# Optimization experiments

Measured on AMD Instinct MI355X. Metric: run time of the kernel, lower is better.

The kernel has to match this reference:

```python
import jax, jax.numpy as jnp
import numpy as np

N = 50000
E = 800000
B = 64
NODE_IN, EDGE_IN, H, OUT_DIM = 16, 8, 64, 2


def _glorot(key, shape):
    fan_in, fan_out = shape[0], shape[-1]
    s = jnp.sqrt(6.0 / (fan_in + fan_out))
    return jax.random.uniform(key, shape, jnp.float32, -s, s)


def setup_inputs() -> dict:
    key = jax.random.key(0)
    ks = jax.random.split(key, 32)
    inp = {
        'x': jax.random.normal(ks[0], (N, NODE_IN), jnp.float32),
        'edge_index': jax.random.randint(ks[1], (2, E), 0, N).astype(jnp.int64),
        'edge_attr': jax.random.normal(ks[2], (E, EDGE_IN), jnp.float32),
        'batch': jnp.sort(jax.random.randint(ks[3], (N,), 0, B)).astype(jnp.int64),
        # encoders
        'W_node': _glorot(ks[4], (NODE_IN, H)), 'b_node': jnp.zeros((H,), jnp.float32),
        'W_edge': _glorot(ks[5], (EDGE_IN, H)), 'b_edge': jnp.zeros((H,), jnp.float32),
        # conv1: GATv2, heads=4, concat=True, edge_dim=H
        'Wl1': _glorot(ks[6], (H, 4 * H)), 'bl1': jnp.zeros((4 * H,), jnp.float32),
        'Wr1': _glorot(ks[7], (H, 4 * H)), 'br1': jnp.zeros((4 * H,), jnp.float32),
        'We1': _glorot(ks[8], (H, 4 * H)),
        'att1': _glorot(ks[9], (4, H)),
        'bias1': jnp.zeros((4 * H,), jnp.float32),
        # conv2: GATv2, heads=1, concat=False, in=4H
        'Wl2': _glorot(ks[10], (4 * H, H)), 'bl2': jnp.zeros((H,), jnp.float32),
        'Wr2': _glorot(ks[11], (4 * H, H)), 'br2': jnp.zeros((H,), jnp.float32),
        'We2': _glorot(ks[12], (H, H)),
        'att2': _glorot(ks[13], (1, H)),
        'bias2': jnp.zeros((H,), jnp.float32),
        # decoder
        'Wd1': _glorot(ks[14], (H, H)), 'bd1': jnp.zeros((H,), jnp.float32),
        'Wd2': _glorot(ks[15], (H, OUT_DIM)), 'bd2': jnp.zeros((OUT_DIM,), jnp.float32),
    }
    return inp


def _gatv2(x, src, dst, eattr, Wl, bl, Wr, br, We, att, bias, heads, out_ch, concat):
    n = x.shape[0]
    # add self-loops with edge_attr fill_value='mean' (segment mean over dst), PyG default
    ones = jnp.ones((src.shape[0],), x.dtype)
    deg = jax.ops.segment_sum(ones, dst, num_segments=n)
    loop_attr = jax.ops.segment_sum(eattr, dst, num_segments=n) / jnp.clip(deg, 1.0)[:, None]
    ea = jnp.concatenate([eattr, loop_attr], 0)               # [E+N, F_e]
    s = jnp.concatenate([src, jnp.arange(n)], 0)
    d = jnp.concatenate([dst, jnp.arange(n)], 0)
    xl = (x @ Wl + bl).reshape(n, heads, out_ch)              # source transform
    xr = (x @ Wr + br).reshape(n, heads, out_ch)              # target transform
    ep = (ea @ We).reshape(-1, heads, out_ch)                 # edge transform (no bias)
    m = jax.nn.leaky_relu(xl[s] + xr[d] + ep, 0.2)            # [E+N, heads, out_ch]
    logits = jnp.einsum('ehc,hc->eh', m, att)
    lmax = jax.ops.segment_max(logits, d, num_segments=n)
    lmax = jnp.where(jnp.isfinite(lmax), lmax, 0.0)
    a = jnp.exp(logits - lmax[d])
    denom = jax.ops.segment_sum(a, d, num_segments=n)
    alpha = a / (denom[d] + 1e-16)                            # segment softmax over dst
    out = jax.ops.segment_sum(alpha[..., None] * xl[s], d, num_segments=n)
    out = out.reshape(n, heads * out_ch) if concat else out.mean(1)
    return out + bias


def reference(x, edge_index, edge_attr, batch, W_node, b_node, W_edge, b_edge,
              Wl1, bl1, Wr1, br1, We1, att1, bias1,
              Wl2, bl2, Wr2, br2, We2, att2, bias2,
              Wd1, bd1, Wd2, bd2):
    src, dst = edge_index[0], edge_index[1]
    h = x @ W_node + b_node
    ea = edge_attr @ W_edge + b_edge
    h = jax.nn.elu(_gatv2(h, src, dst, ea, Wl1, bl1, Wr1, br1, We1, att1, bias1, 4, H, True))
    h = _gatv2(h, src, dst, ea, Wl2, bl2, Wr2, br2, We2, att2, bias2, 1, H, False)
    # global mean pool over batch vector
    cnt = jax.ops.segment_sum(jnp.ones((h.shape[0],), h.dtype), batch, num_segments=B)
    pooled = jax.ops.segment_sum(h, batch, num_segments=B) / jnp.clip(cnt, 1.0)[:, None]
    out = jax.nn.relu(pooled @ Wd1 + bd1) @ Wd2 + bd2
    return jax.nn.sigmoid(out)
```

## Files before the change

kernel.cpp:

```cpp
#include <hip/hip_runtime.h>
#include <math.h>

#define NN 50000
#define NE 800000
#define NB 64

__device__ __forceinline__ int permpos(int c) {
  return ((c & 63) << 2) | (((c >> 6) ^ c) & 3);
}

__device__ __forceinline__ unsigned short f2bf(float f) {
  unsigned int u = __float_as_uint(f);
  u += 0x7fffu + ((u >> 16) & 1u);
  return (unsigned short)(u >> 16);
}
__device__ __forceinline__ float bf2f(unsigned short b) {
  return __uint_as_float(((unsigned int)b) << 16);
}

__global__ void k_zero(int* __restrict__ p, int n) {
  int i = blockIdx.x * blockDim.x + threadIdx.x;
  if (i < n) p[i] = 0;
}

__global__ void k_fuse(const float* __restrict__ Wn, const float* __restrict__ bn,
                       const float* __restrict__ We, const float* __restrict__ be,
                       const float* __restrict__ Wl1, const float* __restrict__ bl1,
                       const float* __restrict__ Wr1, const float* __restrict__ br1,
                       const float* __restrict__ We1, const float* __restrict__ We2,
                       const float* __restrict__ att1, const float* __restrict__ bias1,
                       float* __restrict__ wl1e, float* __restrict__ bl1e,
                       float* __restrict__ wr1e, float* __restrict__ br1e,
                       float* __restrict__ wfe1, float* __restrict__ bfe1,
                       float* __restrict__ wfe2, float* __restrict__ bfe2,
                       float* __restrict__ att1p, float* __restrict__ bias1p) {
  int t = blockIdx.x * blockDim.x + threadIdx.x;
  if (t < 4096) {
    int i = t >> 8, j = t & 255; float s = 0.f;
    for (int k = 0; k < 64; k++) s += Wn[i * 64 + k] * Wl1[k * 256 + j];
    wl1e[i * 256 + permpos(j)] = s;
  } else if (t < 8192) {
    int u = t - 4096; int i = u >> 8, j = u & 255; float s = 0.f;
    for (int k = 0; k < 64; k++) s += Wn[i * 64 + k] * Wr1[k * 256 + j];
    wr1e[i * 256 + permpos(j)] = s;
  } else if (t < 10240) {
    int u = t - 8192; int i = u >> 8, j = u & 255; float s = 0.f;
    for (int k = 0; k < 64; k++) s += We[i * 64 + k] * We1[k * 256 + j];
    wfe1[i * 256 + permpos(j)] = s;
  } else if (t < 10752) {
    int u = t - 10240; int i = u >> 6, j = u & 63; float s = 0.f;
    for (int k = 0; k < 64; k++) s += We[i * 64 + k] * We2[k * 64 + j];
    wfe2[u] = s;
  } else if (t < 11008) {
    int j = t - 10752; float s = bl1[j];
    for (int k = 0; k < 64; k++) s += bn[k] * Wl1[k * 256 + j];
    bl1e[permpos(j)] = s;
  } else if (t < 11264) {
    int j = t - 11008; float s = br1[j];
    for (int k = 0; k < 64; k++) s += bn[k] * Wr1[k * 256 + j];
    br1e[permpos(j)] = s;
  } else if (t < 11520) {
    int j = t - 11264; float s = 0.f;
    for (int k = 0; k < 64; k++) s += be[k] * We1[k * 256 + j];
    bfe1[permpos(j)] = s;
  } else if (t < 11584) {
    int j = t - 11520; float s = 0.f;
    for (int k = 0; k < 64; k++) s += be[k] * We2[k * 64 + j];
    bfe2[j] = s;
  } else if (t < 11840) {
    int j = t - 11584;
    att1p[permpos(j)] = att1[j];
  } else if (t < 12096) {
    int j = t - 11840;
    bias1p[permpos(j)] = bias1[j];
  }
}

__global__ void k_deg(const int* __restrict__ dstA, int* __restrict__ deg) {
  int e = blockIdx.x * blockDim.x + threadIdx.x;
  if (e < NE) atomicAdd(&deg[dstA[e]], 1);
}

__global__ __launch_bounds__(1024) void k_scan1(const int* __restrict__ deg,
                                                int* __restrict__ incl, int* __restrict__ partials) {
  __shared__ int sm[1024];
  int i = blockIdx.x * 1024 + threadIdx.x;
  int v = (i < NN) ? (deg[i] + 1) : 0;
  sm[threadIdx.x] = v;
  __syncthreads();
  for (int off = 1; off < 1024; off <<= 1) {
    int t = (threadIdx.x >= off) ? sm[threadIdx.x - off] : 0;
    __syncthreads();
    sm[threadIdx.x] += t;
    __syncthreads();
  }
  if (i < NN) incl[i] = sm[threadIdx.x];
  if (threadIdx.x == 1023) partials[blockIdx.x] = sm[1023];
}

__global__ void k_scan2(int* __restrict__ partials, int* __restrict__ rowptr, int nblk) {
  int t = threadIdx.x;
  int v = (t < nblk) ? partials[t] : 0;
  for (int off = 1; off < 64; off <<= 1) {
    int u = __shfl_up(v, off, 64);
    if (t >= off) v += u;
  }
  if (t < nblk) partials[t] = v;
  if (t == nblk - 1) rowptr[NN] = v;
}

__global__ void k_scan3(const int* __restrict__ deg, const int* __restrict__ incl,
                        const int* __restrict__ partials, int* __restrict__ rowptr) {
  int i = blockIdx.x * blockDim.x + threadIdx.x;
  if (i >= NN) return;
  int blk = i >> 10;
  int base = blk ? partials[blk - 1] : 0;
  rowptr[i] = base + incl[i] - (deg[i] + 1);
}

__global__ void k_csr(const int* __restrict__ srcA, const int* __restrict__ dstA,
                      const int* __restrict__ rowptr, const int* __restrict__ deg,
                      int* __restrict__ cursor, int2* __restrict__ csr) {
  int t = blockIdx.x * blockDim.x + threadIdx.x;
  if (t < NE) {
    int d = dstA[t];
    int pos = rowptr[d] + atomicAdd(&cursor[d], 1);
    csr[pos] = make_int2(t, srcA[t]);
  } else if (t < NE + NN) {
    int n = t - NE;
    csr[rowptr[n] + deg[n]] = make_int2(NE + n, n);
  }
}

__global__ __launch_bounds__(256) void k_loop8(const int* __restrict__ rowptr,
                                               const int2* __restrict__ csr,
                                               const float* __restrict__ eattr,
                                               float* __restrict__ lattr) {
  int d = (blockIdx.x * blockDim.x + threadIdx.x) >> 6;
  int lane = threadIdx.x & 63;
  if (d >= NN) return;
  int beg = rowptr[d], endReal = rowptr[d + 1] - 1;
  int k = lane & 7, sub = lane >> 3;
  float s = 0.f;
  for (int i = beg + sub; i < endReal; i += 8) {
    int eid = csr[i].x;
    s += eattr[(size_t)eid * 8 + k];
  }
  s += __shfl_xor(s, 8, 64);
  s += __shfl_xor(s, 16, 64);
  s += __shfl_xor(s, 32, 64);
  float invdeg = 1.f / fmaxf((float)(endReal - beg), 1.f);
  if (lane < 8) lattr[(size_t)d * 8 + lane] = s * invdeg;
}

__global__ __launch_bounds__(256) void k_lin1(const float* __restrict__ x,
                                              const float* __restrict__ wl, const float* __restrict__ bl,
                                              const float* __restrict__ wr, const float* __restrict__ br,
                                              unsigned short* __restrict__ xl, float* __restrict__ xr) {
  __shared__ float xs[4][16];
  int nb = blockIdx.x * 4;
  int t = threadIdx.x;
  if (t < 64) xs[t >> 4][t & 15] = x[nb * 16 + t];
  __syncthreads();
  int w = t >> 6, lane = t & 63, l4 = lane << 2;
  float4 accl = *(const float4*)(bl + l4);
  float4 accr = *(const float4*)(br + l4);
  const float* xrow = xs[w];
#pragma unroll
  for (int k = 0; k < 16; k++) {
    float xv = xrow[k];
    float4 wl4 = *(const float4*)(wl + k * 256 + l4);
    float4 wr4 = *(const float4*)(wr + k * 256 + l4);
    accl.x += xv * wl4.x; accl.y += xv * wl4.y; accl.z += xv * wl4.z; accl.w += xv * wl4.w;
    accr.x += xv * wr4.x; accr.y += xv * wr4.y; accr.z += xv * wr4.z; accr.w += xv * wr4.w;
  }
  int node = nb + w;
  ushort4 us;
  us.x = f2bf(accl.x); us.y = f2bf(accl.y); us.z = f2bf(accl.z); us.w = f2bf(accl.w);
  *(ushort4*)(xl + (size_t)node * 256 + l4) = us;
  *(float4*)(xr + (size_t)node * 256 + l4) = accr;
}

__device__ __forceinline__ const float* ek_ptr(const float* __restrict__ eattr,
                                               const float* __restrict__ lattr, int eid) {
  return (eid < NE) ? (eattr + (size_t)eid * 8) : (lattr + (size_t)(eid - NE) * 8);
}

__device__ __forceinline__ float jreduce(float part[4]) {
  part[0] += __shfl_xor(part[1], 1, 64);
  part[2] += __shfl_xor(part[3], 1, 64);
  float v = part[0] + __shfl_xor(part[2], 2, 64);
  v += __shfl_xor(v, 4, 64);
  v += __shfl_xor(v, 8, 64);
  v += __shfl_xor(v, 16, 64);
  v += __shfl_xor(v, 32, 64);
  return v;
}

__global__ __launch_bounds__(256) void k_conv1(
    const float* __restrict__ eattr, const float* __restrict__ lattr,
    const int* __restrict__ rowptr, const int2* __restrict__ csr,
    const unsigned short* __restrict__ xl, const float* __restrict__ xrg,
    const float* __restrict__ att1p, const float* __restrict__ bias1p,
    const float* __restrict__ wfe1, const float* __restrict__ bfe1,
    float* __restrict__ out1) {
  int d = __builtin_amdgcn_readfirstlane((blockIdx.x * blockDim.x + threadIdx.x) >> 6);
  int lane = threadIdx.x & 63;
  if (d >= NN) return;
  int l4 = lane << 2;
  float4 xr4 = *(const float4*)(xrg + (size_t)d * 256 + l4);
  float4 at4 = *(const float4*)(att1p + l4);
  float4 bf4 = *(const float4*)(bfe1 + l4);
  float4 wf[8];
#pragma unroll
  for (int k = 0; k < 8; k++) wf[k] = *(const float4*)(wfe1 + k * 256 + l4);

  float acc0 = 0.f, acc1 = 0.f, acc2 = 0.f, acc3 = 0.f;
  float mrun = -INFINITY, lrun = 0.f;
  int beg = rowptr[d], end = rowptr[d + 1];

  auto ld4 = [&](int s) -> float4 {
    ushort4 u = *(const ushort4*)(xl + (size_t)s * 256 + l4);
    float4 f; f.x = bf2f(u.x); f.y = bf2f(u.y); f.z = bf2f(u.z); f.w = bf2f(u.w);
    return f;
  };
  auto epart = [&](const float* __restrict__ p, const float4& x4, float part[4]) {
    float e0 = bf4.x, e1 = bf4.y, e2 = bf4.z, e3 = bf4.w;
#pragma unroll
    for (int k = 0; k < 8; k++) {
      float ekv = p[k];
      e0 += ekv * wf[k].x; e1 += ekv * wf[k].y;
      e2 += ekv * wf[k].z; e3 += ekv * wf[k].w;
    }
    float m0 = x4.x + xr4.x + e0; m0 = (m0 > 0.f) ? m0 : 0.2f * m0;
    float m1 = x4.y + xr4.y + e1; m1 = (m1 > 0.f) ? m1 : 0.2f * m1;
    float m2 = x4.z + xr4.z + e2; m2 = (m2 > 0.f) ? m2 : 0.2f * m2;
    float m3 = x4.w + xr4.w + e3; m3 = (m3 > 0.f) ? m3 : 0.2f * m3;
    part[0] = at4.x * m0; part[1] = at4.y * m1;
    part[2] = at4.z * m2; part[3] = at4.w * m3;
  };

  int idx = beg;
  for (; idx + 4 <= end; idx += 4) {
    int2 e0 = csr[idx], e1 = csr[idx + 1], e2 = csr[idx + 2], e3 = csr[idx + 3];
    int s0 = __builtin_amdgcn_readfirstlane(e0.y), id0 = __builtin_amdgcn_readfirstlane(e0.x);
    int s1 = __builtin_amdgcn_readfirstlane(e1.y), id1 = __builtin_amdgcn_readfirstlane(e1.x);
    int s2 = __builtin_amdgcn_readfirstlane(e2.y), id2 = __builtin_amdgcn_readfirstlane(e2.x);
    int s3 = __builtin_amdgcn_readfirstlane(e3.y), id3 = __builtin_amdgcn_readfirstlane(e3.x);
    float4 x0 = ld4(s0), x1 = ld4(s1), x2 = ld4(s2), x3 = ld4(s3);
    float pa[4], pb[4], pc[4], pd[4];
    epart(ek_ptr(eattr, lattr, id0), x0, pa);
    epart(ek_ptr(eattr, lattr, id1), x1, pb);
    epart(ek_ptr(eattr, lattr, id2), x2, pc);
    epart(ek_ptr(eattr, lattr, id3), x3, pd);
    float v0 = jreduce(pa), v1 = jreduce(pb), v2 = jreduce(pc), v3 = jreduce(pd);
    float gmax = fmaxf(fmaxf(v0, v1), fmaxf(v2, v3));
    if (__ballot(gmax > mrun)) {
      float nm = fmaxf(mrun, gmax);
      float sc = __expf(mrun - nm);
      mrun = nm; lrun *= sc;
      float sc1 = __shfl_xor(sc, 1, 64);
      float sc2 = __shfl_xor(sc, 2, 64);
      float sc3 = __shfl_xor(sc1, 2, 64);
      acc0 *= sc; acc1 *= sc1; acc2 *= sc2; acc3 *= sc3;
    }
    float q0 = __expf(v0 - mrun), q1 = __expf(v1 - mrun);
    float q2 = __expf(v2 - mrun), q3 = __expf(v3 - mrun);
    lrun += q0 + q1 + q2 + q3;
    {
      float a1 = __shfl_xor(q0, 1, 64), a2 = __shfl_xor(q0, 2, 64), a3 = __shfl_xor(a1, 2, 64);
      acc0 += q0 * x0.x; acc1 += a1 * x0.y; acc2 += a2 * x0.z; acc3 += a3 * x0.w;
    }
    {
      float a1 = __shfl_xor(q1, 1, 64), a2 = __shfl_xor(q1, 2, 64), a3 = __shfl_xor(a1, 2, 64);
      acc0 += q1 * x1.x; acc1 += a1 * x1.y; acc2 += a2 * x1.z; acc3 += a3 * x1.w;
    }
    {
      float a1 = __shfl_xor(q2, 1, 64), a2 = __shfl_xor(q2, 2, 64), a3 = __shfl_xor(a1, 2, 64);
      acc0 += q2 * x2.x; acc1 += a1 * x2.y; acc2 += a2 * x2.z; acc3 += a3 * x2.w;
    }
    {
      float a1 = __shfl_xor(q3, 1, 64), a2 = __shfl_xor(q3, 2, 64), a3 = __shfl_xor(a1, 2, 64);
      acc0 += q3 * x3.x; acc1 += a1 * x3.y; acc2 += a2 * x3.z; acc3 += a3 * x3.w;
    }
  }
  for (; idx < end; ++idx) {
    int2 e0 = csr[idx];
    int s0 = __builtin_amdgcn_readfirstlane(e0.y), id0 = __builtin_amdgcn_readfirstlane(e0.x);
    float4 x0 = ld4(s0);
    float pa[4];
    epart(ek_ptr(eattr, lattr, id0), x0, pa);
    float v0 = jreduce(pa);
    if (__ballot(v0 > mrun)) {
      float nm = fmaxf(mrun, v0);
      float sc = __expf(mrun - nm);
      mrun = nm; lrun *= sc;
      float sc1 = __shfl_xor(sc, 1, 64);
      float sc2 = __shfl_xor(sc, 2, 64);
      float sc3 = __shfl_xor(sc1, 2, 64);
      acc0 *= sc; acc1 *= sc1; acc2 *= sc2; acc3 *= sc3;
    }
    float q0 = __expf(v0 - mrun);
    lrun += q0;
    float a1 = __shfl_xor(q0, 1, 64), a2 = __shfl_xor(q0, 2, 64), a3 = __shfl_xor(a1, 2, 64);
    acc0 += q0 * x0.x; acc1 += a1 * x0.y; acc2 += a2 * x0.z; acc3 += a3 * x0.w;
  }

  float lr0 = lrun;
  float lr1 = __shfl_xor(lr0, 1, 64);
  float lr2 = __shfl_xor(lr0, 2, 64);
  float lr3 = __shfl_xor(lr1, 2, 64);
  float4 bi4 = *(const float4*)(bias1p + l4);
  float4 o;
  o.x = acc0 / (lr0 + 1e-16f) + bi4.x;
  o.y = acc1 / (lr1 + 1e-16f) + bi4.y;
  o.z = acc2 / (lr2 + 1e-16f) + bi4.z;
  o.w = acc3 / (lr3 + 1e-16f) + bi4.w;
  o.x = (o.x > 0.f) ? o.x : (__expf(o.x) - 1.f);
  o.y = (o.y > 0.f) ? o.y : (__expf(o.y) - 1.f);
  o.z = (o.z > 0.f) ? o.z : (__expf(o.z) - 1.f);
  o.w = (o.w > 0.f) ? o.w : (__expf(o.w) - 1.f);
  *(float4*)(out1 + (size_t)d * 256 + l4) = o;
}

__global__ __launch_bounds__(256) void k_lin2(const float* __restrict__ in,
                                              const float* __restrict__ wl, const float* __restrict__ bl,
                                              const float* __restrict__ wr, const float* __restrict__ br,
                                              unsigned short* __restrict__ xl, float* __restrict__ xr) {
  int col = threadIdx.x & 63;
  int grp = threadIdx.x >> 6;
  int node0 = blockIdx.x * 32 + grp * 8;
  float sl[8], sr[8];
  float blv = bl[col], brv = br[col];
#pragma unroll
  for (int u = 0; u < 8; u++) { sl[u] = blv; sr[u] = brv; }
  const float4* r[8];
#pragma unroll
  for (int u = 0; u < 8; u++) r[u] = (const float4*)(in + (size_t)(node0 + u) * 256);
#pragma unroll 2
  for (int g4 = 0; g4 < 64; g4++) {
    int b = g4 & 3;
    int i0 = ((0 ^ b) << 6) + g4;
    int i1 = ((1 ^ b) << 6) + g4;
    int i2 = ((2 ^ b) << 6) + g4;
    int i3 = ((3 ^ b) << 6) + g4;
    float wl0 = wl[i0 * 64 + col], wl1v = wl[i1 * 64 + col];
    float wl2v = wl[i2 * 64 + col], wl3v = wl[i3 * 64 + col];
    float wr0 = wr[i0 * 64 + col], wr1v = wr[i1 * 64 + col];
    float wr2v = wr[i2 * 64 + col], wr3v = wr[i3 * 64 + col];
#pragma unroll
    for (int u = 0; u < 8; u++) {
      float4 v = r[u][g4];
      sl[u] += v.x * wl0 + v.y * wl1v + v.z * wl2v + v.w * wl3v;
      sr[u] += v.x * wr0 + v.y * wr1v + v.z * wr2v + v.w * wr3v;
    }
  }
#pragma unroll
  for (int u = 0; u < 8; u++) {
    int node = node0 + u;
    if (node < NN) {
      xl[(size_t)node * 64 + col] = f2bf(sl[u]);
      xr[(size_t)node * 64 + col] = sr[u];
    }
  }
}

__global__ __launch_bounds__(256) void k_conv2(
    const float* __restrict__ eattr, const float* __restrict__ lattr,
    const int* __restrict__ rowptr, const int2* __restrict__ csr,
    const unsigned short* __restrict__ xl, const float* __restrict__ xrg,
    const float* __restrict__ att2, const float* __restrict__ bias2,
    const float* __restrict__ wfe2, const float* __restrict__ bfe2,
    float* __restrict__ out2) {
  int d = __builtin_amdgcn_readfirstlane((blockIdx.x * blockDim.x + threadIdx.x) >> 6);
  int lane = threadIdx.x & 63;
  if (d >= NN) return;
  float xr_l = xrg[(size_t)d * 64 + lane];
  float att_l = att2[lane];
  float bfe_l = bfe2[lane];
  float wfe_l[8];
#pragma unroll
  for (int k = 0; k < 8; k++) wfe_l[k] = wfe2[k * 64 + lane];
  float acc = 0.f, mrun = -INFINITY, lrun = 0.f;
  int beg = rowptr[d], end = rowptr[d + 1];
  bool b0 = (lane & 1), b1 = (lane & 2);

  auto pl = [&](const float* __restrict__ p, float xs) {
    float ep = bfe_l;
#pragma unroll
    for (int k = 0; k < 8; k++) ep += p[k] * wfe_l[k];
    float m = xs + xr_l + ep;
    m = (m > 0.f) ? m : 0.2f * m;
    return att_l * m;
  };

  int idx = beg;
  for (; idx + 4 <= end; idx += 4) {
    int2 e0 = csr[idx], e1 = csr[idx + 1], e2 = csr[idx + 2], e3 = csr[idx + 3];
    int s0 = __builtin_amdgcn_readfirstlane(e0.y), id0 = __builtin_amdgcn_readfirstlane(e0.x);
    int s1 = __builtin_amdgcn_readfirstlane(e1.y), id1 = __builtin_amdgcn_readfirstlane(e1.x);
    int s2 = __builtin_amdgcn_readfirstlane(e2.y), id2 = __builtin_amdgcn_readfirstlane(e2.x);
    int s3 = __builtin_amdgcn_readfirstlane(e3.y), id3 = __builtin_amdgcn_readfirstlane(e3.x);
    float x0 = bf2f(xl[(size_t)s0 * 64 + lane]);
    float x1 = bf2f(xl[(size_t)s1 * 64 + lane]);
    float x2 = bf2f(xl[(size_t)s2 * 64 + lane]);
    float x3 = bf2f(xl[(size_t)s3 * 64 + lane]);
    float v0 = pl(ek_ptr(eattr, lattr, id0), x0);
    float v1 = pl(ek_ptr(eattr, lattr, id1), x1);
    float v2 = pl(ek_ptr(eattr, lattr, id2), x2);
    float v3 = pl(ek_ptr(eattr, lattr, id3), x3);
    float a01 = b0 ? v1 : v0;
    a01 += __shfl_xor(b0 ? v0 : v1, 1, 64);
    float a23 = b0 ? v3 : v2;
    a23 += __shfl_xor(b0 ? v2 : v3, 1, 64);
    float w = b1 ? a23 : a01;
    w += __shfl_xor(b1 ? a01 : a23, 2, 64);
    w += __shfl_xor(w, 4, 64);
    w += __shfl_xor(w, 8, 64);
    w += __shfl_xor(w, 16, 64);
    w += __shfl_xor(w, 32, 64);
    float g = fmaxf(w, __shfl_xor(w, 1, 64));
    g = fmaxf(g, __shfl_xor(g, 2, 64));
    if (g > mrun) {
      float sc = __expf(mrun - g);
      mrun = g; lrun *= sc; acc *= sc;
    }
    float q = __expf(w - mrun);
    float q1 = __shfl_xor(q, 1, 64);
    float q2 = __shfl_xor(q, 2, 64);
    float q3 = __shfl_xor(q1, 2, 64);
    lrun += (q + q1) + (q2 + q3);
    float u01 = b0 ? x1 : x0, u10 = b0 ? x0 : x1;
    float u23 = b0 ? x3 : x2, u32 = b0 ? x2 : x3;
    float xr0 = b1 ? u23 : u01;
    float xr1v = b1 ? u32 : u10;
    float xr2v = b1 ? u01 : u23;
    float xr3v = b1 ? u10 : u32;
    acc += q * xr0 + q1 * xr1v + q2 * xr2v + q3 * xr3v;
  }
  for (; idx < end; ++idx) {
    int2 e0 = csr[idx];
    int s0 = __builtin_amdgcn_readfirstlane(e0.y), id0 = __builtin_amdgcn_readfirstlane(e0.x);
    float x0 = bf2f(xl[(size_t)s0 * 64 + lane]);
    float v = pl(ek_ptr(eattr, lattr, id0), x0);
    v += __shfl_xor(v, 1, 64);
    v += __shfl_xor(v, 2, 64);
    v += __shfl_xor(v, 4, 64);
    v += __shfl_xor(v, 8, 64);
    v += __shfl_xor(v, 16, 64);
    v += __shfl_xor(v, 32, 64);
    if (v > mrun) {
      float sc = __expf(mrun - v);
      mrun = v; lrun *= sc; acc *= sc;
    }
    float q = __expf(v - mrun);
    lrun += q;
    acc += q * x0;
  }
  out2[(size_t)d * 64 + lane] = acc / (lrun + 1e-16f) + bias2[lane];
}

__device__ __forceinline__ int lowerb(const int* a, int n, int v) {
  int lo = 0, hi = n;
  while (lo < hi) {
    int mid = (lo + hi) >> 1;
    if (a[mid] < v) lo = mid + 1; else hi = mid;
  }
  return lo;
}

__global__ __launch_bounds__(256) void k_pool(const int* __restrict__ batch,
                                              const float* __restrict__ out2,
                                              float* __restrict__ pooled) {
  int b = blockIdx.x;
  int start = lowerb(batch, NN, b);
  int end = lowerb(batch, NN, b + 1);
  int c = threadIdx.x & 63, sub = threadIdx.x >> 6;
  float s = 0.f;
  for (int i = start + sub; i < end; i += 4) s += out2[(size_t)i * 64 + c];
  __shared__ float sm[256];
  sm[threadIdx.x] = s;
  __syncthreads();
  if (sub == 0) {
    float tot = sm[c] + sm[64 + c] + sm[128 + c] + sm[192 + c];
    float cnt = fmaxf((float)(end - start), 1.f);
    pooled[b * 64 + c] = tot / cnt;
  }
}

__global__ __launch_bounds__(1024) void k_dec(const float* __restrict__ pooled,
                                              const float* __restrict__ Wd1, const float* __restrict__ bd1,
                                              const float* __restrict__ Wd2, const float* __restrict__ bd2,
                                              float* __restrict__ out) {
  __shared__ float hid[64 * 64];
  int t = threadIdx.x;
  for (int i = t; i < 4096; i += 1024) {
    int b = i >> 6, j = i & 63;
    float s = bd1[j];
#pragma unroll 8
    for (int k = 0; k < 64; k++) s += pooled[b * 64 + k] * Wd1[k * 64 + j];
    hid[i] = fmaxf(s, 0.f);
  }
  __syncthreads();
  if (t < 128) {
    int b = t >> 1, o = t & 1;
    float s = bd2[o];
#pragma unroll 8
    for (int k = 0; k < 64; k++) s += hid[b * 64 + k] * Wd2[k * 2 + o];
    out[t] = 1.f / (1.f + __expf(-s));
  }
}

extern "C" void kernel_launch(void* const* d_in, const int* in_sizes, int n_in,
                              void* d_out, int out_size, void* d_ws, size_t ws_size,
                              hipStream_t stream) {
  const float* x     = (const float*)d_in[0];
  const int*   eidx  = (const int*)d_in[1];
  const float* eattr = (const float*)d_in[2];
  const int*   batch = (const int*)d_in[3];
  const float* Wn    = (const float*)d_in[4];
  const float* bn    = (const float*)d_in[5];
  const float* We    = (const float*)d_in[6];
  const float* be    = (const float*)d_in[7];
  const float* Wl1   = (const float*)d_in[8];
  const float* bl1   = (const float*)d_in[9];
  const float* Wr1   = (const float*)d_in[10];
  const float* br1   = (const float*)d_in[11];
  const float* We1   = (const float*)d_in[12];
  const float* att1  = (const float*)d_in[13];
  const float* bias1 = (const float*)d_in[14];
  const float* Wl2   = (const float*)d_in[15];
  const float* bl2   = (const float*)d_in[16];
  const float* Wr2   = (const float*)d_in[17];
  const float* br2   = (const float*)d_in[18];
  const float* We2   = (const float*)d_in[19];
  const float* att2  = (const float*)d_in[20];
  const float* bias2 = (const float*)d_in[21];
  const float* Wd1   = (const float*)d_in[22];
  const float* bd1   = (const float*)d_in[23];
  const float* Wd2   = (const float*)d_in[24];
  const float* bd2   = (const float*)d_in[25];

  const int* srcA = eidx;
  const int* dstA = eidx + NE;

  char* ws = (char*)d_ws;
  size_t off = 0;
  auto alloc = [&](size_t bytes) -> char* {
    char* p = ws + off;
    off += (bytes + 255) & ~(size_t)255;
    return p;
  };

  int*   deg    = (int*)alloc(NN * 4);
  int*   cursor = (int*)alloc(NN * 4);
  size_t zero_bytes = off;
  int*   rowptr   = (int*)alloc((NN + 1) * 4);
  int*   incl     = (int*)alloc(NN * 4);
  int*   partials = (int*)alloc(64 * 4);
  int2*  csr      = (int2*)alloc((size_t)(NE + NN + 1) * 8);
  float* lattr = (float*)alloc((size_t)NN * 8 * 4);
  float* wl1e  = (float*)alloc(4096 * 4);
  float* wr1e  = (float*)alloc(4096 * 4);
  float* wfe1  = (float*)alloc(2048 * 4);
  float* wfe2  = (float*)alloc(512 * 4);
  float* bl1e  = (float*)alloc(256 * 4);
  float* br1e  = (float*)alloc(256 * 4);
  float* bfe1  = (float*)alloc(256 * 4);
  float* bfe2  = (float*)alloc(64 * 4);
  float* att1p = (float*)alloc(256 * 4);
  float* bias1p= (float*)alloc(256 * 4);
  unsigned short* xl1 = (unsigned short*)alloc((size_t)NN * 256 * 2);
  float* xr1   = (float*)alloc((size_t)NN * 256 * 4);
  float* out1  = (float*)alloc((size_t)NN * 256 * 4);
  unsigned short* xl2 = (unsigned short*)alloc((size_t)NN * 64 * 2);
  float* xr2   = (float*)alloc((size_t)NN * 64 * 4);
  float* out2  = (float*)alloc((size_t)NN * 64 * 4);
  float* pooled = (float*)alloc((size_t)NB * 64 * 4);

  int zn = (int)(zero_bytes / 4);
  int nscan = (NN + 1023) / 1024;
  k_zero<<<(zn + 255) / 256, 256, 0, stream>>>((int*)d_ws, zn);
  k_fuse<<<(12096 + 255) / 256, 256, 0, stream>>>(Wn, bn, We, be, Wl1, bl1, Wr1, br1, We1, We2,
                                                  att1, bias1,
                                                  wl1e, bl1e, wr1e, br1e, wfe1, bfe1, wfe2, bfe2,
                                                  att1p, bias1p);
  k_deg<<<(NE + 255) / 256, 256, 0, stream>>>(dstA, deg);
  k_scan1<<<nscan, 1024, 0, stream>>>(deg, incl, partials);
  k_scan2<<<1, 64, 0, stream>>>(partials, rowptr, nscan);
  k_scan3<<<(NN + 255) / 256, 256, 0, stream>>>(deg, incl, partials, rowptr);
  k_csr<<<(NE + NN + 255) / 256, 256, 0, stream>>>(srcA, dstA, rowptr, deg, cursor, csr);
  k_loop8<<<(NN + 3) / 4, 256, 0, stream>>>(rowptr, csr, eattr, lattr);
  k_lin1<<<NN / 4, 256, 0, stream>>>(x, wl1e, bl1e, wr1e, br1e, xl1, xr1);
  k_conv1<<<(NN + 3) / 4, 256, 0, stream>>>(eattr, lattr, rowptr, csr, xl1, xr1,
                                            att1p, bias1p, wfe1, bfe1, out1);
  k_lin2<<<(NN + 31) / 32, 256, 0, stream>>>(out1, Wl2, bl2, Wr2, br2, xl2, xr2);
  k_conv2<<<(NN + 3) / 4, 256, 0, stream>>>(eattr, lattr, rowptr, csr, xl2, xr2,
                                            att2, bias2, wfe2, bfe2, out2);
  k_pool<<<NB, 256, 0, stream>>>(batch, out2, pooled);
  k_dec<<<1, 1024, 0, stream>>>(pooled, Wd1, bd1, Wd2, bd2, (float*)d_out);
}
```

Baseline: 771.7 us.

## Split GATv2 convs into per-edge logit kernels and per-node softmax aggregation

Attention logits are now computed in separate edge-parallel kernels (one wave per four CSR entries, reading a new per-position dst array) and written to buffers. The per-node aggregation kernels then only read precomputed logits plus gathered source features. This is meant to spread the heavy per-edge work evenly instead of binding it to skewed per-node loops. Edge biases are folded into the right-projection biases, and attention vectors are pre-scaled by log2(e) so exp2f can be used. The cost is extra logit and dst buffers, plus a second gather of x_l in the logit pass.

Result: slower. 894.4 us (+15.9%).

```diff
diff --git a/kernel.cpp b/kernel.cpp
--- a/kernel.cpp
+++ b/kernel.cpp
@@ -4,6 +4,8 @@
 #define NN 50000
 #define NE 800000
 #define NB 64
+#define TOT 850000
+#define LOG2E 1.4426950408889634f
 
 __device__ __forceinline__ int permpos(int c) {
   return ((c & 63) << 2) | (((c >> 6) ^ c) & 3);
@@ -29,11 +31,13 @@
                        const float* __restrict__ Wr1, const float* __restrict__ br1,
                        const float* __restrict__ We1, const float* __restrict__ We2,
                        const float* __restrict__ att1, const float* __restrict__ bias1,
+                       const float* __restrict__ att2,
                        float* __restrict__ wl1e, float* __restrict__ bl1e,
                        float* __restrict__ wr1e, float* __restrict__ br1e,
-                       float* __restrict__ wfe1, float* __restrict__ bfe1,
-                       float* __restrict__ wfe2, float* __restrict__ bfe2,
-                       float* __restrict__ att1p, float* __restrict__ bias1p) {
+                       float* __restrict__ wfe1, float* __restrict__ wfe2,
+                       float* __restrict__ bfe2,
+                       float* __restrict__ att1p, float* __restrict__ att2p,
+                       float* __restrict__ bias1p) {
   int t = blockIdx.x * blockDim.x + threadIdx.x;
   if (t < 4096) {
     int i = t >> 8, j = t & 255; float s = 0.f;
@@ -58,20 +62,20 @@
   } else if (t < 11264) {
     int j = t - 11008; float s = br1[j];
     for (int k = 0; k < 64; k++) s += bn[k] * Wr1[k * 256 + j];
+    for (int k = 0; k < 64; k++) s += be[k] * We1[k * 256 + j];
     br1e[permpos(j)] = s;
-  } else if (t < 11520) {
+  } else if (t < 11328) {
     int j = t - 11264; float s = 0.f;
-    for (int k = 0; k < 64; k++) s += be[k] * We1[k * 256 + j];
-    bfe1[permpos(j)] = s;
-  } else if (t < 11584) {
-    int j = t - 11520; float s = 0.f;
     for (int k = 0; k < 64; k++) s += be[k] * We2[k * 64 + j];
     bfe2[j] = s;
-  } else if (t < 11840) {
+  } else if (t < 11584) {
+    int j = t - 11328;
+    att1p[permpos(j)] = att1[j] * LOG2E;
+  } else if (t < 11648) {
     int j = t - 11584;
-    att1p[permpos(j)] = att1[j];
-  } else if (t < 12096) {
-    int j = t - 11840;
+    att2p[j] = att2[j] * LOG2E;
+  } else if (t < 11904) {
+    int j = t - 11648;
     bias1p[permpos(j)] = bias1[j];
   }
 }
@@ -120,15 +124,19 @@
 
 __global__ void k_csr(const int* __restrict__ srcA, const int* __restrict__ dstA,
                       const int* __restrict__ rowptr, const int* __restrict__ deg,
-                      int* __restrict__ cursor, int2* __restrict__ csr) {
+                      int* __restrict__ cursor, int2* __restrict__ csr,
+                      int* __restrict__ dstp) {
   int t = blockIdx.x * blockDim.x + threadIdx.x;
   if (t < NE) {
     int d = dstA[t];
     int pos = rowptr[d] + atomicAdd(&cursor[d], 1);
     csr[pos] = make_int2(t, srcA[t]);
+    dstp[pos] = d;
   } else if (t < NE + NN) {
     int n = t - NE;
-    csr[rowptr[n] + deg[n]] = make_int2(NE + n, n);
+    int pos = rowptr[n] + deg[n];
+    csr[pos] = make_int2(NE + n, n);
+    dstp[pos] = n;
   }
 }
 
@@ -197,24 +205,66 @@
   return v;
 }
 
-__global__ __launch_bounds__(256) void k_conv1(
+__global__ __launch_bounds__(256) void k_elogit1(
     const float* __restrict__ eattr, const float* __restrict__ lattr,
+    const int2* __restrict__ csr, const int* __restrict__ dstp,
+    const unsigned short* __restrict__ xl, const float* __restrict__ xrb,
+    const float* __restrict__ att1p, const float* __restrict__ wfe1,
+    float* __restrict__ logit1) {
+  int wid = (blockIdx.x * blockDim.x + threadIdx.x) >> 6;
+  int lane = threadIdx.x & 63;
+  int p0 = wid * 4;
+  int l4 = lane << 2;
+  float4 at4 = *(const float4*)(att1p + l4);
+  float4 wf[8];
+#pragma unroll
+  for (int k = 0; k < 8; k++) wf[k] = *(const float4*)(wfe1 + k * 256 + l4);
+  float v[4];
+#pragma unroll
+  for (int i = 0; i < 4; i++) {
+    int p = p0 + i;
+    int2 e = csr[p];
+    int eid = __builtin_amdgcn_readfirstlane(e.x);
+    int s   = __builtin_amdgcn_readfirstlane(e.y);
+    int dd  = __builtin_amdgcn_readfirstlane(dstp[p]);
+    const float* ekp = ek_ptr(eattr, lattr, eid);
+    float4 xb = *(const float4*)(xrb + (size_t)dd * 256 + l4);
+    ushort4 u = *(const ushort4*)(xl + (size_t)s * 256 + l4);
+    float m0 = xb.x + bf2f(u.x);
+    float m1 = xb.y + bf2f(u.y);
+    float m2 = xb.z + bf2f(u.z);
+    float m3 = xb.w + bf2f(u.w);
+#pragma unroll
+    for (int k = 0; k < 8; k++) {
+      float ekv = ekp[k];
+      m0 += ekv * wf[k].x; m1 += ekv * wf[k].y;
+      m2 += ekv * wf[k].z; m3 += ekv * wf[k].w;
+    }
+    m0 = (m0 > 0.f) ? m0 : 0.2f * m0;
+    m1 = (m1 > 0.f) ? m1 : 0.2f * m1;
+    m2 = (m2 > 0.f) ? m2 : 0.2f * m2;
+    m3 = (m3 > 0.f) ? m3 : 0.2f * m3;
+    float part[4] = {at4.x * m0, at4.y * m1, at4.z * m2, at4.w * m3};
+    v[i] = jreduce(part);
+  }
+  int key = (lane >> 2) & 3;
+  float a = (key & 1) ? v[1] : v[0];
+  float b = (key & 1) ? v[3] : v[2];
+  float out = (key & 2) ? b : a;
+  if (lane < 16) logit1[(size_t)p0 * 4 + lane] = out;
+}
+
+__global__ __launch_bounds__(256) void k_conv1l(
     const int* __restrict__ rowptr, const int2* __restrict__ csr,
-    const unsigned short* __restrict__ xl, const float* __restrict__ xrg,
-    const float* __restrict__ att1p, const float* __restrict__ bias1p,
-    const float* __restrict__ wfe1, const float* __restrict__ bfe1,
+    const float* __restrict__ logit1,
+    const unsigned short* __restrict__ xl,
+    const float* __restrict__ bias1p,
     float* __restrict__ out1) {
   int d = __builtin_amdgcn_readfirstlane((blockIdx.x * blockDim.x + threadIdx.x) >> 6);
   int lane = threadIdx.x & 63;
   if (d >= NN) return;
   int l4 = lane << 2;
-  float4 xr4 = *(const float4*)(xrg + (size_t)d * 256 + l4);
-  float4 at4 = *(const float4*)(att1p + l4);
-  float4 bf4 = *(const float4*)(bfe1 + l4);
-  float4 wf[8];
-#pragma unroll
-  for (int k = 0; k < 8; k++) wf[k] = *(const float4*)(wfe1 + k * 256 + l4);
-
+  int k = lane & 3;
   float acc0 = 0.f, acc1 = 0.f, acc2 = 0.f, acc3 = 0.f;
   float mrun = -INFINITY, lrun = 0.f;
   int beg = rowptr[d], end = rowptr[d + 1];
@@ -224,49 +274,36 @@
     float4 f; f.x = bf2f(u.x); f.y = bf2f(u.y); f.z = bf2f(u.z); f.w = bf2f(u.w);
     return f;
   };
-  auto epart = [&](const float* __restrict__ p, const float4& x4, float part[4]) {
-    float e0 = bf4.x, e1 = bf4.y, e2 = bf4.z, e3 = bf4.w;
-#pragma unroll
-    for (int k = 0; k < 8; k++) {
-      float ekv = p[k];
-      e0 += ekv * wf[k].x; e1 += ekv * wf[k].y;
-      e2 += ekv * wf[k].z; e3 += ekv * wf[k].w;
-    }
-    float m0 = x4.x + xr4.x + e0; m0 = (m0 > 0.f) ? m0 : 0.2f * m0;
-    float m1 = x4.y + xr4.y + e1; m1 = (m1 > 0.f) ? m1 : 0.2f * m1;
-    float m2 = x4.z + xr4.z + e2; m2 = (m2 > 0.f) ? m2 : 0.2f * m2;
-    float m3 = x4.w + xr4.w + e3; m3 = (m3 > 0.f) ? m3 : 0.2f * m3;
-    part[0] = at4.x * m0; part[1] = at4.y * m1;
-    part[2] = at4.z * m2; part[3] = at4.w * m3;
+  auto sel = [&](const float4& lg) -> float {
+    float a = (k & 1) ? lg.y : lg.x;
+    float b = (k & 1) ? lg.w : lg.z;
+    return (k & 2) ? b : a;
   };
 
   int idx = beg;
   for (; idx + 4 <= end; idx += 4) {
     int2 e0 = csr[idx], e1 = csr[idx + 1], e2 = csr[idx + 2], e3 = csr[idx + 3];
-    int s0 = __builtin_amdgcn_readfirstlane(e0.y), id0 = __builtin_amdgcn_readfirstlane(e0.x);
-    int s1 = __builtin_amdgcn_readfirstlane(e1.y), id1 = __builtin_amdgcn_readfirstlane(e1.x);
-    int s2 = __builtin_amdgcn_readfirstlane(e2.y), id2 = __builtin_amdgcn_readfirstlane(e2.x);
-    int s3 = __builtin_amdgcn_readfirstlane(e3.y), id3 = __builtin_amdgcn_readfirstlane(e3.x);
+    int s0 = __builtin_amdgcn_readfirstlane(e0.y);
+    int s1 = __builtin_amdgcn_readfirstlane(e1.y);
+    int s2 = __builtin_amdgcn_readfirstlane(e2.y);
+    int s3 = __builtin_amdgcn_readfirstlane(e3.y);
+    const float4* lgp = (const float4*)(logit1 + (size_t)idx * 4);
+    float4 lg0 = lgp[0], lg1 = lgp[1], lg2 = lgp[2], lg3 = lgp[3];
+    float v0 = sel(lg0), v1 = sel(lg1), v2 = sel(lg2), v3 = sel(lg3);
     float4 x0 = ld4(s0), x1 = ld4(s1), x2 = ld4(s2), x3 = ld4(s3);
-    float pa[4], pb[4], pc[4], pd[4];
-    epart(ek_ptr(eattr, lattr, id0), x0, pa);
-    epart(ek_ptr(eattr, lattr, id1), x1, pb);
-    epart(ek_ptr(eattr, lattr, id2), x2, pc);
-    epart(ek_ptr(eattr, lattr, id3), x3, pd);
-    float v0 = jreduce(pa), v1 = jreduce(pb), v2 = jreduce(pc), v3 = jreduce(pd);
     float gmax = fmaxf(fmaxf(v0, v1), fmaxf(v2, v3));
     if (__ballot(gmax > mrun)) {
       float nm = fmaxf(mrun, gmax);
-      float sc = __expf(mrun - nm);
+      float sc = exp2f(mrun - nm);
       mrun = nm; lrun *= sc;
       float sc1 = __shfl_xor(sc, 1, 64);
       float sc2 = __shfl_xor(sc, 2, 64);
       float sc3 = __shfl_xor(sc1, 2, 64);
       acc0 *= sc; acc1 *= sc1; acc2 *= sc2; acc3 *= sc3;
     }
-    float q0 = __expf(v0 - mrun), q1 = __expf(v1 - mrun);
-    float q2 = __expf(v2 - mrun), q3 = __expf(v3 - mrun);
-    lrun += q0 + q1 + q2 + q3;
+    float q0 = exp2f(v0 - mrun), q1 = exp2f(v1 - mrun);
+    float q2 = exp2f(v2 - mrun), q3 = exp2f(v3 - mrun);
+    lrun += (q0 + q1) + (q2 + q3);
     {
       float a1 = __shfl_xor(q0, 1, 64), a2 = __shfl_xor(q0, 2, 64), a3 = __shfl_xor(a1, 2, 64);
       acc0 += q0 * x0.x; acc1 += a1 * x0.y; acc2 += a2 * x0.z; acc3 += a3 * x0.w;
@@ -286,21 +323,20 @@
   }
   for (; idx < end; ++idx) {
     int2 e0 = csr[idx];
-    int s0 = __builtin_amdgcn_readfirstlane(e0.y), id0 = __builtin_amdgcn_readfirstlane(e0.x);
+    int s0 = __builtin_amdgcn_readfirstlane(e0.y);
+    float4 lg0 = *(const float4*)(logit1 + (size_t)idx * 4);
+    float v0 = sel(lg0);
     float4 x0 = ld4(s0);
-    float pa[4];
-    epart(ek_ptr(eattr, lattr, id0), x0, pa);
-    float v0 = jreduce(pa);
     if (__ballot(v0 > mrun)) {
       float nm = fmaxf(mrun, v0);
-      float sc = __expf(mrun - nm);
+      float sc = exp2f(mrun - nm);
       mrun = nm; lrun *= sc;
       float sc1 = __shfl_xor(sc, 1, 64);
       float sc2 = __shfl_xor(sc, 2, 64);
       float sc3 = __shfl_xor(sc1, 2, 64);
       acc0 *= sc; acc1 *= sc1; acc2 *= sc2; acc3 *= sc3;
     }
-    float q0 = __expf(v0 - mrun);
+    float q0 = exp2f(v0 - mrun);
     lrun += q0;
     float a1 = __shfl_xor(q0, 1, 64), a2 = __shfl_xor(q0, 2, 64), a3 = __shfl_xor(a1, 2, 64);
     acc0 += q0 * x0.x; acc1 += a1 * x0.y; acc2 += a2 * x0.z; acc3 += a3 * x0.w;
@@ -326,12 +362,13 @@
 __global__ __launch_bounds__(256) void k_lin2(const float* __restrict__ in,
                                               const float* __restrict__ wl, const float* __restrict__ bl,
                                               const float* __restrict__ wr, const float* __restrict__ br,
+                                              const float* __restrict__ bfe2,
                                               unsigned short* __restrict__ xl, float* __restrict__ xr) {
   int col = threadIdx.x & 63;
   int grp = threadIdx.x >> 6;
   int node0 = blockIdx.x * 32 + grp * 8;
   float sl[8], sr[8];
-  float blv = bl[col], brv = br[col];
+  float blv = bl[col], brv = br[col] + bfe2[col];
 #pragma unroll
   for (int u = 0; u < 8; u++) { sl[u] = blv; sr[u] = brv; }
   const float4* r[8];
@@ -365,95 +402,92 @@
   }
 }
 
-__global__ __launch_bounds__(256) void k_conv2(
+__global__ __launch_bounds__(256) void k_elogit2(
     const float* __restrict__ eattr, const float* __restrict__ lattr,
+    const int2* __restrict__ csr, const int* __restrict__ dstp,
+    const unsigned short* __restrict__ xl, const float* __restrict__ xrb,
+    const float* __restrict__ att2p, const float* __restrict__ wfe2,
+    float* __restrict__ logit2) {
+  int wid = (blockIdx.x * blockDim.x + threadIdx.x) >> 6;
+  int lane = threadIdx.x & 63;
+  int p0 = wid * 4;
+  float att_l = att2p[lane];
+  float wfe_l[8];
+#pragma unroll
+  for (int k = 0; k < 8; k++) wfe_l[k] = wfe2[k * 64 + lane];
+  float v[4];
+#pragma unroll
+  for (int i = 0; i < 4; i++) {
+    int p = p0 + i;
+    int2 e = csr[p];
+    int eid = __builtin_amdgcn_readfirstlane(e.x);
+    int s   = __builtin_amdgcn_readfirstlane(e.y);
+    int dd  = __builtin_amdgcn_readfirstlane(dstp[p]);
+    const float* ekp = ek_ptr(eattr, lattr, eid);
+    float m = xrb[(size_t)dd * 64 + lane] + bf2f(xl[(size_t)s * 64 + lane]);
+#pragma unroll
+    for (int k = 0; k < 8; k++) m += ekp[k] * wfe_l[k];
+    m = (m > 0.f) ? m : 0.2f * m;
+    float t = att_l * m;
+    t += __shfl_xor(t, 1, 64);
+    t += __shfl_xor(t, 2, 64);
+    t += __shfl_xor(t, 4, 64);
+    t += __shfl_xor(t, 8, 64);
+    t += __shfl_xor(t, 16, 64);
+    t += __shfl_xor(t, 32, 64);
+    v[i] = t;
+  }
+  int key = lane & 3;
+  float a = (key & 1) ? v[1] : v[0];
+  float b = (key & 1) ? v[3] : v[2];
+  float out = (key & 2) ? b : a;
+  if (lane < 4) logit2[p0 + lane] = out;
+}
+
+__global__ __launch_bounds__(256) void k_conv2l(
     const int* __restrict__ rowptr, const int2* __restrict__ csr,
-    const unsigned short* __restrict__ xl, const float* __restrict__ xrg,
-    const float* __restrict__ att2, const float* __restrict__ bias2,
-    const float* __restrict__ wfe2, const float* __restrict__ bfe2,
+    const float* __restrict__ logit2,
+    const unsigned short* __restrict__ xl,
+    const float* __restrict__ bias2,
     float* __restrict__ out2) {
   int d = __builtin_amdgcn_readfirstlane((blockIdx.x * blockDim.x + threadIdx.x) >> 6);
   int lane = threadIdx.x & 63;
   if (d >= NN) return;
-  float xr_l = xrg[(size_t)d * 64 + lane];
-  float att_l = att2[lane];
-  float bfe_l = bfe2[lane];
-  float wfe_l[8];
-#pragma unroll
-  for (int k = 0; k < 8; k++) wfe_l[k] = wfe2[k * 64 + lane];
   float acc = 0.f, mrun = -INFINITY, lrun = 0.f;
   int beg = rowptr[d], end = rowptr[d + 1];
-  bool b0 = (lane & 1), b1 = (lane & 2);
-
-  auto pl = [&](const float* __restrict__ p, float xs) {
-    float ep = bfe_l;
-#pragma unroll
-    for (int k = 0; k < 8; k++) ep += p[k] * wfe_l[k];
-    float m = xs + xr_l + ep;
-    m = (m > 0.f) ? m : 0.2f * m;
-    return att_l * m;
-  };
 
   int idx = beg;
   for (; idx + 4 <= end; idx += 4) {
     int2 e0 = csr[idx], e1 = csr[idx + 1], e2 = csr[idx + 2], e3 = csr[idx + 3];
-    int s0 = __builtin_amdgcn_readfirstlane(e0.y), id0 = __builtin_amdgcn_readfirstlane(e0.x);
-    int s1 = __builtin_amdgcn_readfirstlane(e1.y), id1 = __builtin_amdgcn_readfirstlane(e1.x);
-    int s2 = __builtin_amdgcn_readfirstlane(e2.y), id2 = __builtin_amdgcn_readfirstlane(e2.x);
-    int s3 = __builtin_amdgcn_readfirstlane(e3.y), id3 = __builtin_amdgcn_readfirstlane(e3.x);
+    int s0 = __builtin_amdgcn_readfirstlane(e0.y);
+    int s1 = __builtin_amdgcn_readfirstlane(e1.y);
+    int s2 = __builtin_amdgcn_readfirstlane(e2.y);
+    int s3 = __builtin_amdgcn_readfirstlane(e3.y);
+    float l0 = logit2[idx], l1 = logit2[idx + 1], l2 = logit2[idx + 2], l3 = logit2[idx + 3];
     float x0 = bf2f(xl[(size_t)s0 * 64 + lane]);
     float x1 = bf2f(xl[(size_t)s1 * 64 + lane]);
     float x2 = bf2f(xl[(size_t)s2 * 64 + lane]);
     float x3 = bf2f(xl[(size_t)s3 * 64 + lane]);
-    float v0 = pl(ek_ptr(eattr, lattr, id0), x0);
-    float v1 = pl(ek_ptr(eattr, lattr, id1), x1);
-    float v2 = pl(ek_ptr(eattr, lattr, id2), x2);
-    float v3 = pl(ek_ptr(eattr, lattr, id3), x3);
-    float a01 = b0 ? v1 : v0;
-    a01 += __shfl_xor(b0 ? v0 : v1, 1, 64);
-    float a23 = b0 ? v3 : v2;
-    a23 += __shfl_xor(b0 ? v2 : v3, 1, 64);
-    float w = b1 ? a23 : a01;
-    w += __shfl_xor(b1 ? a01 : a23, 2, 64);
-    w += __shfl_xor(w, 4, 64);
-    w += __shfl_xor(w, 8, 64);
-    w += __shfl_xor(w, 16, 64);
-    w += __shfl_xor(w, 32, 64);
-    float g = fmaxf(w, __shfl_xor(w, 1, 64));
-    g = fmaxf(g, __shfl_xor(g, 2, 64));
+    float g = fmaxf(fmaxf(l0, l1), fmaxf(l2, l3));
     if (g > mrun) {
-      float sc = __expf(mrun - g);
+      float sc = exp2f(mrun - g);
       mrun = g; lrun *= sc; acc *= sc;
     }
-    float q = __expf(w - mrun);
-    float q1 = __shfl_xor(q, 1, 64);
-    float q2 = __shfl_xor(q, 2, 64);
-    float q3 = __shfl_xor(q1, 2, 64);
-    lrun += (q + q1) + (q2 + q3);
-    float u01 = b0 ? x1 : x0, u10 = b0 ? x0 : x1;
-    float u23 = b0 ? x3 : x2, u32 = b0 ? x2 : x3;
-    float xr0 = b1 ? u23 : u01;
-    float xr1v = b1 ? u32 : u10;
-    float xr2v = b1 ? u01 : u23;
-    float xr3v = b1 ? u10 : u32;
-    acc += q * xr0 + q1 * xr1v + q2 * xr2v + q3 * xr3v;
+    float q0 = exp2f(l0 - mrun), q1 = exp2f(l1 - mrun);
+    float q2 = exp2f(l2 - mrun), q3 = exp2f(l3 - mrun);
+    lrun += (q0 + q1) + (q2 + q3);
+    acc += q0 * x0 + q1 * x1 + q2 * x2 + q3 * x3;
   }
   for (; idx < end; ++idx) {
     int2 e0 = csr[idx];
-    int s0 = __builtin_amdgcn_readfirstlane(e0.y), id0 = __builtin_amdgcn_readfirstlane(e0.x);
+    int s0 = __builtin_amdgcn_readfirstlane(e0.y);
+    float l0 = logit2[idx];
     float x0 = bf2f(xl[(size_t)s0 * 64 + lane]);
-    float v = pl(ek_ptr(eattr, lattr, id0), x0);
-    v += __shfl_xor(v, 1, 64);
-    v += __shfl_xor(v, 2, 64);
-    v += __shfl_xor(v, 4, 64);
-    v += __shfl_xor(v, 8, 64);
-    v += __shfl_xor(v, 16, 64);
-    v += __shfl_xor(v, 32, 64);
-    if (v > mrun) {
-      float sc = __expf(mrun - v);
-      mrun = v; lrun *= sc; acc *= sc;
-    }
-    float q = __expf(v - mrun);
+    if (l0 > mrun) {
+      float sc = exp2f(mrun - l0);
+      mrun = l0; lrun *= sc; acc *= sc;
+    }
+    float q = exp2f(l0 - mrun);
     lrun += q;
     acc += q * x0;
   }
@@ -558,7 +592,8 @@
   int*   rowptr   = (int*)alloc((NN + 1) * 4);
   int*   incl     = (int*)alloc(NN * 4);
   int*   partials = (int*)alloc(64 * 4);
-  int2*  csr      = (int2*)alloc((size_t)(NE + NN + 1) * 8);
+  int2*  csr      = (int2*)alloc((size_t)(TOT + 1) * 8);
+  int*   dstp     = (int*)alloc((size_t)TOT * 4);
   float* lattr = (float*)alloc((size_t)NN * 8 * 4);
   float* wl1e  = (float*)alloc(4096 * 4);
   float* wr1e  = (float*)alloc(4096 * 4);
@@ -566,37 +601,40 @@
   float* wfe2  = (float*)alloc(512 * 4);
   float* bl1e  = (float*)alloc(256 * 4);
   float* br1e  = (float*)alloc(256 * 4);
-  float* bfe1  = (float*)alloc(256 * 4);
   float* bfe2  = (float*)alloc(64 * 4);
   float* att1p = (float*)alloc(256 * 4);
+  float* att2p = (float*)alloc(64 * 4);
   float* bias1p= (float*)alloc(256 * 4);
   unsigned short* xl1 = (unsigned short*)alloc((size_t)NN * 256 * 2);
-  float* xr1   = (float*)alloc((size_t)NN * 256 * 4);
+  float* xrb1  = (float*)alloc((size_t)NN * 256 * 4);
   float* out1  = (float*)alloc((size_t)NN * 256 * 4);
   unsigned short* xl2 = (unsigned short*)alloc((size_t)NN * 64 * 2);
-  float* xr2   = (float*)alloc((size_t)NN * 64 * 4);
+  float* xrb2  = (float*)alloc((size_t)NN * 64 * 4);
   float* out2  = (float*)alloc((size_t)NN * 64 * 4);
+  float* logit1 = (float*)alloc((size_t)TOT * 4 * 4);
+  float* logit2 = (float*)alloc((size_t)TOT * 4);
   float* pooled = (float*)alloc((size_t)NB * 64 * 4);
 
   int zn = (int)(zero_bytes / 4);
   int nscan = (NN + 1023) / 1024;
+  int nelog = TOT / 16;
   k_zero<<<(zn + 255) / 256, 256, 0, stream>>>((int*)d_ws, zn);
-  k_fuse<<<(12096 + 255) / 256, 256, 0, stream>>>(Wn, bn, We, be, Wl1, bl1, Wr1, br1, We1, We2,
-                                                  att1, bias1,
-                                                  wl1e, bl1e, wr1e, br1e, wfe1, bfe1, wfe2, bfe2,
-                                                  att1p, bias1p);
+  k_fuse<<<(11904 + 255) / 256, 256, 0, stream>>>(Wn, bn, We, be, Wl1, bl1, Wr1, br1, We1, We2,
+                                                  att1, bias1, att2,
+                                                  wl1e, bl1e, wr1e, br1e, wfe1, wfe2, bfe2,
+                                                  att1p, att2p, bias1p);
   k_deg<<<(NE + 255) / 256, 256, 0, stream>>>(dstA, deg);
   k_scan1<<<nscan, 1024, 0, stream>>>(deg, incl, partials);
   k_scan2<<<1, 64, 0, stream>>>(partials, rowptr, nscan);
   k_scan3<<<(NN + 255) / 256, 256, 0, stream>>>(deg, incl, partials, rowptr);
-  k_csr<<<(NE + NN + 255) / 256, 256, 0, stream>>>(srcA, dstA, rowptr, deg, cursor, csr);
+  k_csr<<<(NE + NN + 255) / 256, 256, 0, stream>>>(srcA, dstA, rowptr, deg, cursor, csr, dstp);
   k_loop8<<<(NN + 3) / 4, 256, 0, stream>>>(rowptr, csr, eattr, lattr);
-  k_lin1<<<NN / 4, 256, 0, stream>>>(x, wl1e, bl1e, wr1e, br1e, xl1, xr1);
-  k_conv1<<<(NN + 3) / 4, 256, 0, stream>>>(eattr, lattr, rowptr, csr, xl1, xr1,
-                                            att1p, bias1p, wfe1, bfe1, out1);
-  k_lin2<<<(NN + 31) / 32, 256, 0, stream>>>(out1, Wl2, bl2, Wr2, br2, xl2, xr2);
-  k_conv2<<<(NN + 3) / 4, 256, 0, stream>>>(eattr, lattr, rowptr, csr, xl2, xr2,
-                                            att2, bias2, wfe2, bfe2, out2);
+  k_lin1<<<NN / 4, 256, 0, stream>>>(x, wl1e, bl1e, wr1e, br1e, xl1, xrb1);
+  k_elogit1<<<nelog, 256, 0, stream>>>(eattr, lattr, csr, dstp, xl1, xrb1, att1p, wfe1, logit1);
+  k_conv1l<<<(NN + 3) / 4, 256, 0, stream>>>(rowptr, csr, logit1, xl1, bias1p, out1);
+  k_lin2<<<(NN + 31) / 32, 256, 0, stream>>>(out1, Wl2, bl2, Wr2, br2, bfe2, xl2, xrb2);
+  k_elogit2<<<nelog, 256, 0, stream>>>(eattr, lattr, csr, dstp, xl2, xrb2, att2p, wfe2, logit2);
+  k_conv2l<<<(NN + 3) / 4, 256, 0, stream>>>(rowptr, csr, logit2, xl2, bias2, out2);
   k_pool<<<NB, 256, 0, stream>>>(batch, out2, pooled);
   k_dec<<<1, 1024, 0, stream>>>(pooled, Wd1, bd1, Wd2, bd2, (float*)d_out);
 }
```
